# Performance work log

Measured on AMD Instinct MI355X. Metric: run time of the kernel, lower is better.

The kernel has to match this reference:

```python
import jax, jax.numpy as jnp
import numpy as np

TOP_K = 4  # router top-k


def setup_inputs() -> dict:
    key = jax.random.key(0)
    ks = jax.random.split(key, 8)
    B, S, D, E, H, HS = 2, 2048, 2048, 16, 1024, 4096
    scaled = lambda k, shape, fan: (jax.random.normal(k, shape, jnp.float32) * (fan ** -0.5))
    return {
        "x": jax.random.normal(ks[0], (B, S, D), jnp.float32),
        "w_router": scaled(ks[1], (D, E), D),
        # per-expert SwiGLU MLP weights
        "we1": scaled(ks[2], (E, D, H), D),
        "we3": scaled(ks[3], (E, D, H), D),
        "we2": scaled(ks[4], (E, H, D), H),
        # shared SwiGLU MLP weights
        "ws1": scaled(ks[5], (D, HS), D),
        "ws3": scaled(ks[6], (D, HS), D),
        "ws2": scaled(ks[7], (HS, D), HS),
    }


def reference(x, w_router, we1, we3, we2, ws1, ws3, ws2):
    B, S, D = x.shape
    T = B * S
    E = w_router.shape[1]
    xt = x.reshape(T, D)

    # ---- router: softmax over experts, top-k, renormalize top-k weights ----
    probs = jax.nn.softmax(xt @ w_router, axis=-1)           # [T, E]
    top_w, top_i = jax.lax.top_k(probs, TOP_K)               # [T, K]
    top_w = top_w / jnp.sum(top_w, axis=-1, keepdims=True)
    # dense combine weights [T, E] (zero for non-selected experts)
    cw = jnp.zeros((T, E), xt.dtype).at[jnp.arange(T)[:, None], top_i].add(top_w)

    # ---- experts: per-expert SwiGLU, combine with routing weights ----
    g = jax.nn.silu(jnp.einsum("td,edh->teh", xt, we1)) * jnp.einsum("td,edh->teh", xt, we3)
    g = g * cw[:, :, None]                                   # fold combine weight in
    moe_out = jnp.einsum("teh,ehd->td", g, we2)              # [T, D]

    # ---- shared MLP (SwiGLU) and blend ----
    shared = (jax.nn.silu(xt @ ws1) * (xt @ ws3)) @ ws2      # [T, D]
    k = TOP_K
    out = shared / (k + 1) + moe_out * (k / (k + 1))
    return out.reshape(B, S, D)
```

## Files before the change

### kernel.cpp

```cpp
#include <hip/hip_runtime.h>
#include <stdint.h>

#define TTOK  4096
#define DDIM  2048
#define NEXP  16
#define HDIM  1024
#define HSDIM 4096
#define CAPR  18432

typedef __bf16 bf16x8 __attribute__((ext_vector_type(8)));
typedef float  f32x4  __attribute__((ext_vector_type(4)));

__device__ __forceinline__ unsigned short f2b(float f) {
  union { float f; unsigned int i; } v; v.f = f;
  unsigned int r = (v.i + 0x7fffu + ((v.i >> 16) & 1u)) >> 16;
  return (unsigned short)r;
}
__device__ __forceinline__ float b2f(unsigned short u) {
  union { unsigned int i; float f; } v; v.i = ((unsigned int)u) << 16; return v.f;
}
__device__ __forceinline__ float silu_f(float x) { return x / (1.f + __expf(-x)); }

__device__ __forceinline__ void gload16(const void* g, void* l) {
  __builtin_amdgcn_global_load_lds(
      (const __attribute__((address_space(1))) unsigned int*)(uintptr_t)g,
      (__attribute__((address_space(3))) unsigned int*)(uintptr_t)l,
      16, 0, 0);
}

__global__ void cvt_bf16_kernel(const float* __restrict__ in, unsigned short* __restrict__ out, int n8) {
  int i = blockIdx.x * 256 + threadIdx.x;
  if (i >= n8) return;
  const float4* p = (const float4*)in + (size_t)i * 2;
  float4 a = p[0], b = p[1];
  uint4 o;
  o.x = (unsigned)f2b(a.x) | ((unsigned)f2b(a.y) << 16);
  o.y = (unsigned)f2b(a.z) | ((unsigned)f2b(a.w) << 16);
  o.z = (unsigned)f2b(b.x) | ((unsigned)f2b(b.y) << 16);
  o.w = (unsigned)f2b(b.z) | ((unsigned)f2b(b.w) << 16);
  ((uint4*)out)[i] = o;
}

__global__ void transpose_f2b(const float* __restrict__ in, unsigned short* __restrict__ out, int R, int C) {
  __shared__ unsigned short t[64][66];
  size_t zo = (size_t)blockIdx.z * R * C;
  int c0 = blockIdx.x * 64, r0 = blockIdx.y * 64;
  int x = threadIdx.x & 63, y = threadIdx.x >> 6;
#pragma unroll
  for (int j = 0; j < 16; ++j) {
    int r = y * 16 + j;
    t[x][r] = f2b(in[zo + (size_t)(r0 + r) * C + c0 + x]);
  }
  __syncthreads();
#pragma unroll
  for (int j = 0; j < 16; ++j) {
    int c = y * 16 + j;
    out[zo + (size_t)(c0 + c) * R + r0 + x] = t[c][x];
  }
}

__global__ __launch_bounds__(256) void router_kernel(const float* __restrict__ x, const float* __restrict__ wr,
                                                     float* __restrict__ topw, int* __restrict__ topi) {
  int tok = blockIdx.x * 4 + (threadIdx.x >> 6);
  int lane = threadIdx.x & 63;
  const float* xr = x + (size_t)tok * DDIM;
  float acc[NEXP];
#pragma unroll
  for (int e = 0; e < NEXP; ++e) acc[e] = 0.f;
  for (int it = 0; it < DDIM / 64; ++it) {
    int d = it * 64 + lane;
    float xv = xr[d];
    const float4* w4 = (const float4*)(wr + (size_t)d * NEXP);
    float4 w0 = w4[0], w1 = w4[1], w2 = w4[2], w3 = w4[3];
    acc[0] += xv * w0.x; acc[1] += xv * w0.y; acc[2] += xv * w0.z; acc[3] += xv * w0.w;
    acc[4] += xv * w1.x; acc[5] += xv * w1.y; acc[6] += xv * w1.z; acc[7] += xv * w1.w;
    acc[8] += xv * w2.x; acc[9] += xv * w2.y; acc[10] += xv * w2.z; acc[11] += xv * w2.w;
    acc[12] += xv * w3.x; acc[13] += xv * w3.y; acc[14] += xv * w3.z; acc[15] += xv * w3.w;
  }
#pragma unroll
  for (int e = 0; e < NEXP; ++e) {
#pragma unroll
    for (int off = 32; off > 0; off >>= 1) acc[e] += __shfl_xor(acc[e], off);
  }
  unsigned used = 0u;
  float lv[4]; int si[4];
#pragma unroll
  for (int k = 0; k < 4; ++k) {
    float best = -3.4e38f; int bi = 0;
    for (int e = 0; e < NEXP; ++e) {
      if (!((used >> e) & 1u) && acc[e] > best) { best = acc[e]; bi = e; }
    }
    used |= 1u << bi; lv[k] = best; si[k] = bi;
  }
  if (lane == 0) {
    float m = lv[0], s = 0.f, w[4];
#pragma unroll
    for (int k = 0; k < 4; ++k) { w[k] = __expf(lv[k] - m); s += w[k]; }
    float inv = 1.f / s;
#pragma unroll
    for (int k = 0; k < 4; ++k) { topw[tok * 4 + k] = w[k] * inv; topi[tok * 4 + k] = si[k]; }
  }
}

__global__ void zero_kernel(int* b) { if (threadIdx.x < 64) b[threadIdx.x] = 0; }

__global__ void count_kernel(const int* __restrict__ topi, int* counts, int n) {
  int i = blockIdx.x * 256 + threadIdx.x;
  if (i < n) atomicAdd(&counts[topi[i]], 1);
}

__global__ void offsets_kernel(const int* counts, int* eoff) {
  if (threadIdx.x == 0 && blockIdx.x == 0) {
    int o = 0;
    for (int e = 0; e < NEXP; ++e) { eoff[e] = o; o += (counts[e] + 127) & ~127; }
    eoff[NEXP] = o;
  }
}

__global__ void prefill_kernel(int* gtok, float* gwt, int cap) {
  int i = blockIdx.x * 256 + threadIdx.x;
  if (i < cap) { gtok[i] = 0; gwt[i] = 0.f; }
}

__global__ void scatter_kernel(const int* __restrict__ topi, const float* __restrict__ topw,
                               const int* __restrict__ eoff, int* cursors,
                               int* gtok, float* gwt, int* posmap, int n) {
  int i = blockIdx.x * 256 + threadIdx.x;
  if (i >= n) return;
  int e = topi[i];
  int pos = eoff[e] + atomicAdd(&cursors[e], 1);
  gtok[pos] = i >> 2;
  gwt[pos] = topw[i] * 0.8f;
  posmap[i] = pos;
}

__global__ void silu_mul_kernel(const unsigned short* __restrict__ a, const unsigned short* __restrict__ b,
                                unsigned short* __restrict__ g, int n8) {
  int i = blockIdx.x * 256 + threadIdx.x;
  if (i >= n8) return;
  uint4 va = ((const uint4*)a)[i];
  uint4 vb = ((const uint4*)b)[i];
  uint4 vo;
  unsigned* pa = (unsigned*)&va; unsigned* pb = (unsigned*)&vb; unsigned* po = (unsigned*)&vo;
#pragma unroll
  for (int w = 0; w < 4; ++w) {
    float a0 = b2f((unsigned short)(pa[w] & 0xffffu)), a1 = b2f((unsigned short)(pa[w] >> 16));
    float b0 = b2f((unsigned short)(pb[w] & 0xffffu)), b1 = b2f((unsigned short)(pb[w] >> 16));
    float g0 = silu_f(a0) * b0, g1 = silu_f(a1) * b1;
    po[w] = (unsigned)f2b(g0) | ((unsigned)f2b(g1) << 16);
  }
  ((uint4*)g)[i] = vo;
}

__global__ void silu_mul_w_kernel(const unsigned short* __restrict__ a, const unsigned short* __restrict__ b,
                                  const float* __restrict__ gw, unsigned short* __restrict__ g, int n8) {
  int i = blockIdx.x * 256 + threadIdx.x;
  if (i >= n8) return;
  float wrow = gw[i >> 7];
  uint4 va = ((const uint4*)a)[i];
  uint4 vb = ((const uint4*)b)[i];
  uint4 vo;
  unsigned* pa = (unsigned*)&va; unsigned* pb = (unsigned*)&vb; unsigned* po = (unsigned*)&vo;
#pragma unroll
  for (int w = 0; w < 4; ++w) {
    float a0 = b2f((unsigned short)(pa[w] & 0xffffu)), a1 = b2f((unsigned short)(pa[w] >> 16));
    float b0 = b2f((unsigned short)(pb[w] & 0xffffu)), b1 = b2f((unsigned short)(pb[w] >> 16));
    float g0 = silu_f(a0) * b0 * wrow, g1 = silu_f(a1) * b1 * wrow;
    po[w] = (unsigned)f2b(g0) | ((unsigned)f2b(g1) << 16);
  }
  ((uint4*)g)[i] = vo;
}

__global__ __launch_bounds__(256) void combine_kernel(const unsigned short* __restrict__ ecout,
                                                      const int* __restrict__ posmap,
                                                      float* __restrict__ out, int n8) {
  int i = blockIdx.x * 256 + threadIdx.x;
  if (i >= n8) return;
  int t = i >> 8;
  int c = i & 255;
  int4 pv = *(const int4*)&posmap[t * 4];
  float s[8];
  float4 o0 = ((const float4*)out)[(size_t)i * 2];
  float4 o1 = ((const float4*)out)[(size_t)i * 2 + 1];
  s[0]=o0.x; s[1]=o0.y; s[2]=o0.z; s[3]=o0.w; s[4]=o1.x; s[5]=o1.y; s[6]=o1.z; s[7]=o1.w;
  int pos[4] = {pv.x, pv.y, pv.z, pv.w};
#pragma unroll
  for (int k = 0; k < 4; ++k) {
    uint4 v = ((const uint4*)(ecout + (size_t)pos[k] * DDIM))[c];
    unsigned* pw = (unsigned*)&v;
#pragma unroll
    for (int w = 0; w < 4; ++w) {
      s[w * 2]     += b2f((unsigned short)(pw[w] & 0xffffu));
      s[w * 2 + 1] += b2f((unsigned short)(pw[w] >> 16));
    }
  }
  float4 r0 = {s[0], s[1], s[2], s[3]}, r1 = {s[4], s[5], s[6], s[7]};
  ((float4*)out)[(size_t)i * 2] = r0;
  ((float4*)out)[(size_t)i * 2 + 1] = r1;
}

template <int MODE>
__global__ __launch_bounds__(256) void gemm_bt(const unsigned short* __restrict__ A,
                                               const unsigned short* __restrict__ Bt,
                                               unsigned short* __restrict__ Cbf,
                                               float* __restrict__ Cf,
                                               int N, int K,
                                               const int* __restrict__ gtok,
                                               const int* __restrict__ eoff,
                                               float scale) {
  __shared__ unsigned short sA[128 * 64];
  __shared__ unsigned short sB[128 * 64];
  __shared__ int sIdx[128];

  int m0 = blockIdx.x * 128;
  int n0 = blockIdx.y * 128;
  const unsigned short* Bte = Bt;
  if constexpr (MODE == 2 || MODE == 4) {
    if (m0 >= eoff[NEXP]) return;
    int e = 0;
    while (m0 >= eoff[e + 1]) ++e;
    Bte = Bt + (size_t)e * N * K;
  }
  int tid = threadIdx.x;
  int lane = tid & 63;
  int wv = tid >> 6;
  if constexpr (MODE == 2) {
    if (tid < 128) sIdx[tid] = gtok[m0 + tid];
    __syncthreads();
  }
  f32x4 acc[4][4];
#pragma unroll
  for (int mi = 0; mi < 4; ++mi)
#pragma unroll
    for (int ni = 0; ni < 4; ++ni) acc[mi][ni] = (f32x4){0.f, 0.f, 0.f, 0.f};

  int wm = wv >> 1, wn = wv & 1;

  for (int kt = 0; kt < K; kt += 64) {
#pragma unroll
    for (int c = 0; c < 4; ++c) {
      int bofs = (wv * 4 + c) * 1024 + lane * 16;
      int row = bofs >> 7;
      int sch = ((bofs >> 4) & 7) ^ (row & 7);
      int ar;
      if constexpr (MODE == 2) ar = sIdx[row]; else ar = m0 + row;
      gload16(A + (size_t)ar * K + kt + sch * 8, &sA[(wv * 4 + c) * 512]);
      gload16(Bte + (size_t)(n0 + row) * K + kt + sch * 8, &sB[(wv * 4 + c) * 512]);
    }
    __syncthreads();
#pragma unroll
    for (int kk = 0; kk < 2; ++kk) {
      bf16x8 af[4], bfv[4];
#pragma unroll
      for (int mi = 0; mi < 4; ++mi) {
        int row = wm * 64 + mi * 16 + (lane & 15);
        int ch = (kk * 4 + (lane >> 4)) ^ (row & 7);
        af[mi] = *(const bf16x8*)&sA[row * 64 + ch * 8];
      }
#pragma unroll
      for (int ni = 0; ni < 4; ++ni) {
        int row = wn * 64 + ni * 16 + (lane & 15);
        int ch = (kk * 4 + (lane >> 4)) ^ (row & 7);
        bfv[ni] = *(const bf16x8*)&sB[row * 64 + ch * 8];
      }
#pragma unroll
      for (int mi = 0; mi < 4; ++mi)
#pragma unroll
        for (int ni = 0; ni < 4; ++ni)
          acc[mi][ni] = __builtin_amdgcn_mfma_f32_16x16x32_bf16(af[mi], bfv[ni], acc[mi][ni], 0, 0, 0);
    }
    __syncthreads();
  }

#pragma unroll
  for (int mi = 0; mi < 4; ++mi) {
#pragma unroll
    for (int ni = 0; ni < 4; ++ni) {
      int cc = n0 + wn * 64 + ni * 16 + (lane & 15);
#pragma unroll
      for (int j = 0; j < 4; ++j) {
        int rr = m0 + wm * 64 + mi * 16 + ((lane >> 4) << 2) + j;
        float v = acc[mi][ni][j];
        if constexpr (MODE == 1) {
          Cf[(size_t)rr * N + cc] = v * scale;
        } else {
          Cbf[(size_t)rr * N + cc] = f2b(v);
        }
      }
    }
  }
}

extern "C" void kernel_launch(void* const* d_in, const int* in_sizes, int n_in,
                              void* d_out, int out_size, void* d_ws, size_t ws_size,
                              hipStream_t stream) {
  const float* x   = (const float*)d_in[0];
  const float* wr  = (const float*)d_in[1];
  const float* we1 = (const float*)d_in[2];
  const float* we3 = (const float*)d_in[3];
  const float* we2 = (const float*)d_in[4];
  const float* ws1 = (const float*)d_in[5];
  const float* ws3 = (const float*)d_in[6];
  const float* ws2 = (const float*)d_in[7];
  float* out = (float*)d_out;

  char* p = (char*)d_ws;
  auto take = [&](size_t bytes) { char* r = p; p += (bytes + 255) & ~(size_t)255; return r; };
  unsigned short* xbf = (unsigned short*)take((size_t)TTOK * DDIM * 2);
  unsigned short* eh1 = (unsigned short*)take((size_t)CAPR * HDIM * 2);
  unsigned short* h1  = (unsigned short*)take((size_t)TTOK * HSDIM * 2);
  unsigned short* h3  = (unsigned short*)take((size_t)TTOK * HSDIM * 2);
  unsigned short* eh3 = (unsigned short*)take((size_t)CAPR * HDIM * 2);
  unsigned short* tw  = (unsigned short*)take((size_t)NEXP * HDIM * DDIM * 2);
  float* topw = (float*)take((size_t)TTOK * 4 * 4);
  int*   topi = (int*)take((size_t)TTOK * 4 * 4);
  int*   gtok = (int*)take((size_t)CAPR * 4);
  float* gwt  = (float*)take((size_t)CAPR * 4);
  int*   posmap = (int*)take((size_t)TTOK * 4 * 4);
  int*   ibuf = (int*)take(256);
  if ((size_t)(p - (char*)d_ws) > ws_size) return;

  unsigned short* ecout = h1;

  int* counts  = ibuf;
  int* cursors = ibuf + 16;
  int* eoff    = ibuf + 32;

  cvt_bf16_kernel<<<TTOK * DDIM / 8 / 256, 256, 0, stream>>>(x, xbf, TTOK * DDIM / 8);
  router_kernel<<<TTOK / 4, 256, 0, stream>>>(x, wr, topw, topi);
  zero_kernel<<<1, 64, 0, stream>>>(ibuf);
  count_kernel<<<TTOK * 4 / 256, 256, 0, stream>>>(topi, counts, TTOK * 4);
  offsets_kernel<<<1, 64, 0, stream>>>(counts, eoff);
  prefill_kernel<<<CAPR / 256, 256, 0, stream>>>(gtok, gwt, CAPR);
  scatter_kernel<<<TTOK * 4 / 256, 256, 0, stream>>>(topi, topw, eoff, cursors, gtok, gwt, posmap, TTOK * 4);

  transpose_f2b<<<dim3(HSDIM / 64, DDIM / 64, 1), 256, 0, stream>>>(ws1, tw, DDIM, HSDIM);
  gemm_bt<0><<<dim3(TTOK / 128, HSDIM / 128), 256, 0, stream>>>(xbf, tw, h1, nullptr, HSDIM, DDIM, nullptr, nullptr, 0.f);
  transpose_f2b<<<dim3(HSDIM / 64, DDIM / 64, 1), 256, 0, stream>>>(ws3, tw, DDIM, HSDIM);
  gemm_bt<0><<<dim3(TTOK / 128, HSDIM / 128), 256, 0, stream>>>(xbf, tw, h3, nullptr, HSDIM, DDIM, nullptr, nullptr, 0.f);
  silu_mul_kernel<<<TTOK * HSDIM / 8 / 256, 256, 0, stream>>>(h1, h3, h1, TTOK * HSDIM / 8);
  transpose_f2b<<<dim3(DDIM / 64, HSDIM / 64, 1), 256, 0, stream>>>(ws2, tw, HSDIM, DDIM);
  gemm_bt<1><<<dim3(TTOK / 128, DDIM / 128), 256, 0, stream>>>(h1, tw, nullptr, out, DDIM, HSDIM, nullptr, nullptr, 0.2f);

  transpose_f2b<<<dim3(HDIM / 64, DDIM / 64, NEXP), 256, 0, stream>>>(we1, tw, DDIM, HDIM);
  gemm_bt<2><<<dim3(CAPR / 128, HDIM / 128), 256, 0, stream>>>(xbf, tw, eh1, nullptr, HDIM, DDIM, gtok, eoff, 0.f);
  transpose_f2b<<<dim3(HDIM / 64, DDIM / 64, NEXP), 256, 0, stream>>>(we3, tw, DDIM, HDIM);
  gemm_bt<2><<<dim3(CAPR / 128, HDIM / 128), 256, 0, stream>>>(xbf, tw, eh3, nullptr, HDIM, DDIM, gtok, eoff, 0.f);
  silu_mul_w_kernel<<<CAPR * HDIM / 8 / 256, 256, 0, stream>>>(eh1, eh3, gwt, eh1, CAPR * HDIM / 8);
  transpose_f2b<<<dim3(DDIM / 64, HDIM / 64, NEXP), 256, 0, stream>>>(we2, tw, HDIM, DDIM);
  gemm_bt<4><<<dim3(CAPR / 128, DDIM / 128), 256, 0, stream>>>(eh1, tw, ecout, nullptr, DDIM, HDIM, nullptr, eoff, 0.f);

  combine_kernel<<<TTOK * DDIM / 8 / 256, 256, 0, stream>>>(ecout, posmap, out, TTOK * DDIM / 8);
}
```

Baseline: 939.0 us.

## Replace 128x128 GEMM with double-buffered 256x256 pipelined MFMA kernel

Swaps the single-buffered 128x128-tile GEMM for a 256x256-tile, 512-thread kernel. It double-buffers LDS, interleaves async global-to-LDS loads with MFMA phases using explicit waitcnt, barriers and setprio, and remaps workgroups across XCDs. Expert capacity padding grows to 256-row multiples, so the grouped-GEMM buffers are enlarged. The aim is to hide memory latency and raise per-tile data reuse. The cost is more padded expert rows, higher register and LDS pressure, and fragile hand-tuned scheduling.

```diff
diff --git a/kernel.cpp b/kernel.cpp
--- a/kernel.cpp
+++ b/kernel.cpp
@@ -6,7 +6,7 @@
 #define NEXP  16
 #define HDIM  1024
 #define HSDIM 4096
-#define CAPR  18432
+#define CAPR2 20480
 
 typedef __bf16 bf16x8 __attribute__((ext_vector_type(8)));
 typedef float  f32x4  __attribute__((ext_vector_type(4)));
@@ -112,7 +112,7 @@
 __global__ void offsets_kernel(const int* counts, int* eoff) {
   if (threadIdx.x == 0 && blockIdx.x == 0) {
     int o = 0;
-    for (int e = 0; e < NEXP; ++e) { eoff[e] = o; o += (counts[e] + 127) & ~127; }
+    for (int e = 0; e < NEXP; ++e) { eoff[e] = o; o += (counts[e] + 255) & ~255; }
     eoff[NEXP] = o;
   }
 }
@@ -199,96 +199,138 @@
   ((float4*)out)[(size_t)i * 2 + 1] = r1;
 }
 
+
+#define STAGE_A(b, h, kt) do { \
+  gload16(Aptr + (size_t)rA[h][0]*K + (size_t)(kt)*64 + schEl, (char*)sA[b] + (h)*16384 + wv*1024); \
+  gload16(Aptr + (size_t)rA[h][1]*K + (size_t)(kt)*64 + schEl, (char*)sA[b] + (h)*16384 + 8192 + wv*1024); \
+} while (0)
+
+#define STAGE_B(b, h, kt) do { \
+  gload16(Bte + (size_t)rB[h][0]*K + (size_t)(kt)*64 + schEl, (char*)sB[b] + (h)*16384 + wv*1024); \
+  gload16(Bte + (size_t)rB[h][1]*K + (size_t)(kt)*64 + schEl, (char*)sB[b] + (h)*16384 + 8192 + wv*1024); \
+} while (0)
+
+#define PHASE(QA, QB, BUF, VM, ...) do { \
+  bf16x8 af[4][2], bfr[2][2]; \
+  _Pragma("unroll") for (int mi = 0; mi < 4; ++mi) { \
+    const int row_ = (QA)*128 + wr*64 + mi*16 + (lane & 15); \
+    _Pragma("unroll") for (int kk = 0; kk < 2; ++kk) { \
+      const int ch_ = (kk*4 + (lane>>4)) ^ (row_ & 7); \
+      af[mi][kk] = *(const bf16x8*)&sA[BUF][row_*64 + ch_*8]; } } \
+  _Pragma("unroll") for (int ni = 0; ni < 2; ++ni) { \
+    const int row_ = (QB)*128 + wc*32 + ni*16 + (lane & 15); \
+    _Pragma("unroll") for (int kk = 0; kk < 2; ++kk) { \
+      const int ch_ = (kk*4 + (lane>>4)) ^ (row_ & 7); \
+      bfr[ni][kk] = *(const bf16x8*)&sB[BUF][row_*64 + ch_*8]; } } \
+  __VA_ARGS__ \
+  if ((VM) == 4) { asm volatile("s_waitcnt vmcnt(4)" ::: "memory"); } \
+  else if ((VM) == 0) { asm volatile("s_waitcnt vmcnt(0)" ::: "memory"); } \
+  __builtin_amdgcn_sched_barrier(0); \
+  __builtin_amdgcn_s_barrier(); \
+  __builtin_amdgcn_sched_barrier(0); \
+  __builtin_amdgcn_s_setprio(1); \
+  _Pragma("unroll") for (int mi = 0; mi < 4; ++mi) \
+    _Pragma("unroll") for (int ni = 0; ni < 2; ++ni) \
+      _Pragma("unroll") for (int kk = 0; kk < 2; ++kk) \
+        acc[QA][QB][mi][ni] = __builtin_amdgcn_mfma_f32_16x16x32_bf16(af[mi][kk], bfr[ni][kk], acc[QA][QB][mi][ni], 0, 0, 0); \
+  __builtin_amdgcn_s_setprio(0); \
+  __builtin_amdgcn_sched_barrier(0); \
+  __builtin_amdgcn_s_barrier(); \
+  __builtin_amdgcn_sched_barrier(0); \
+} while (0)
+
 template <int MODE>
-__global__ __launch_bounds__(256) void gemm_bt(const unsigned short* __restrict__ A,
-                                               const unsigned short* __restrict__ Bt,
-                                               unsigned short* __restrict__ Cbf,
-                                               float* __restrict__ Cf,
-                                               int N, int K,
-                                               const int* __restrict__ gtok,
-                                               const int* __restrict__ eoff,
-                                               float scale) {
-  __shared__ unsigned short sA[128 * 64];
-  __shared__ unsigned short sB[128 * 64];
-  __shared__ int sIdx[128];
-
-  int m0 = blockIdx.x * 128;
-  int n0 = blockIdx.y * 128;
+__global__ __launch_bounds__(512, 2) void gemm256(const unsigned short* __restrict__ Aptr,
+                                                  const unsigned short* __restrict__ Bt,
+                                                  unsigned short* __restrict__ Cbf,
+                                                  float* __restrict__ Cf,
+                                                  int N, int K, int MB,
+                                                  const int* __restrict__ gtok,
+                                                  const int* __restrict__ eoff,
+                                                  float scale) {
+  __shared__ unsigned short sA[2][256 * 64];
+  __shared__ unsigned short sB[2][256 * 64];
+
+  int nwg = gridDim.x;
+  int q = nwg >> 3, r = nwg & 7;
+  int xcd = blockIdx.x & 7, off = blockIdx.x >> 3;
+  int wg = (xcd < r ? xcd * (q + 1) : r * (q + 1) + (xcd - r) * q) + off;
+  int m0 = (wg % MB) * 256;
+  int n0 = (wg / MB) * 256;
+
   const unsigned short* Bte = Bt;
   if constexpr (MODE == 2 || MODE == 4) {
     if (m0 >= eoff[NEXP]) return;
     int e = 0;
     while (m0 >= eoff[e + 1]) ++e;
-    Bte = Bt + (size_t)e * N * K;
-  }
-  int tid = threadIdx.x;
-  int lane = tid & 63;
-  int wv = tid >> 6;
-  if constexpr (MODE == 2) {
-    if (tid < 128) sIdx[tid] = gtok[m0 + tid];
-    __syncthreads();
-  }
-  f32x4 acc[4][4];
-#pragma unroll
-  for (int mi = 0; mi < 4; ++mi)
-#pragma unroll
-    for (int ni = 0; ni < 4; ++ni) acc[mi][ni] = (f32x4){0.f, 0.f, 0.f, 0.f};
-
-  int wm = wv >> 1, wn = wv & 1;
-
-  for (int kt = 0; kt < K; kt += 64) {
-#pragma unroll
-    for (int c = 0; c < 4; ++c) {
-      int bofs = (wv * 4 + c) * 1024 + lane * 16;
-      int row = bofs >> 7;
-      int sch = ((bofs >> 4) & 7) ^ (row & 7);
-      int ar;
-      if constexpr (MODE == 2) ar = sIdx[row]; else ar = m0 + row;
-      gload16(A + (size_t)ar * K + kt + sch * 8, &sA[(wv * 4 + c) * 512]);
-      gload16(Bte + (size_t)(n0 + row) * K + kt + sch * 8, &sB[(wv * 4 + c) * 512]);
+    Bte += (size_t)e * N * K;
+  }
+
+  int tid = threadIdx.x, lane = tid & 63, wv = tid >> 6;
+  int wr = wv >> 2, wc = wv & 3;
+  const int schEl = ((lane & 7) ^ (lane >> 3)) * 8;
+  int rA[2][2], rB[2][2];
+#pragma unroll
+  for (int h = 0; h < 2; ++h)
+#pragma unroll
+    for (int s = 0; s < 2; ++s) {
+      int row = h * 128 + s * 64 + wv * 8 + (lane >> 3);
+      rB[h][s] = n0 + row;
+      if constexpr (MODE == 2) rA[h][s] = gtok[m0 + row];
+      else rA[h][s] = m0 + row;
     }
-    __syncthreads();
-#pragma unroll
-    for (int kk = 0; kk < 2; ++kk) {
-      bf16x8 af[4], bfv[4];
-#pragma unroll
-      for (int mi = 0; mi < 4; ++mi) {
-        int row = wm * 64 + mi * 16 + (lane & 15);
-        int ch = (kk * 4 + (lane >> 4)) ^ (row & 7);
-        af[mi] = *(const bf16x8*)&sA[row * 64 + ch * 8];
-      }
-#pragma unroll
-      for (int ni = 0; ni < 4; ++ni) {
-        int row = wn * 64 + ni * 16 + (lane & 15);
-        int ch = (kk * 4 + (lane >> 4)) ^ (row & 7);
-        bfv[ni] = *(const bf16x8*)&sB[row * 64 + ch * 8];
-      }
+
+  f32x4 acc[2][2][4][2];
+#pragma unroll
+  for (int a_ = 0; a_ < 2; ++a_)
+#pragma unroll
+    for (int b_ = 0; b_ < 2; ++b_)
 #pragma unroll
       for (int mi = 0; mi < 4; ++mi)
 #pragma unroll
-        for (int ni = 0; ni < 4; ++ni)
-          acc[mi][ni] = __builtin_amdgcn_mfma_f32_16x16x32_bf16(af[mi], bfv[ni], acc[mi][ni], 0, 0, 0);
-    }
-    __syncthreads();
-  }
-
-#pragma unroll
-  for (int mi = 0; mi < 4; ++mi) {
-#pragma unroll
-    for (int ni = 0; ni < 4; ++ni) {
-      int cc = n0 + wn * 64 + ni * 16 + (lane & 15);
-#pragma unroll
-      for (int j = 0; j < 4; ++j) {
-        int rr = m0 + wm * 64 + mi * 16 + ((lane >> 4) << 2) + j;
-        float v = acc[mi][ni][j];
-        if constexpr (MODE == 1) {
-          Cf[(size_t)rr * N + cc] = v * scale;
-        } else {
-          Cbf[(size_t)rr * N + cc] = f2b(v);
+        for (int ni = 0; ni < 2; ++ni) acc[a_][b_][mi][ni] = (f32x4){0.f, 0.f, 0.f, 0.f};
+
+  STAGE_A(0, 0, 0); STAGE_B(0, 0, 0); STAGE_A(0, 1, 0); STAGE_B(0, 1, 0);
+  __builtin_amdgcn_sched_barrier(0);
+  STAGE_A(1, 0, 1); STAGE_B(1, 0, 1); STAGE_A(1, 1, 1); STAGE_B(1, 1, 1);
+  asm volatile("s_waitcnt vmcnt(8)" ::: "memory");
+  __builtin_amdgcn_sched_barrier(0);
+  __builtin_amdgcn_s_barrier();
+  __builtin_amdgcn_sched_barrier(0);
+
+  int NI = K >> 7;
+  for (int j = 0; j < NI; ++j) {
+    int kt1 = 2 * j + 1;
+    bool pre = (j + 1 < NI), post = (j > 0);
+    int vmTail = pre ? 4 : 0;
+    PHASE(0, 0, 0, -1, if (post) { STAGE_A(1, 1, kt1); STAGE_B(1, 1, kt1); });
+    PHASE(0, 1, 0, -1, ;);
+    PHASE(1, 0, 0, -1, if (pre) { STAGE_A(0, 0, kt1 + 1); });
+    PHASE(1, 1, 0, vmTail, if (pre) { STAGE_B(0, 0, kt1 + 1); });
+    PHASE(0, 0, 1, -1, if (pre) { STAGE_A(0, 1, kt1 + 1); STAGE_B(0, 1, kt1 + 1); });
+    PHASE(0, 1, 1, -1, ;);
+    PHASE(1, 0, 1, -1, if (pre) { STAGE_A(1, 0, kt1 + 2); });
+    PHASE(1, 1, 1, vmTail, if (pre) { STAGE_B(1, 0, kt1 + 2); });
+  }
+
+  asm volatile("" ::: "memory");
+#pragma unroll
+  for (int qa = 0; qa < 2; ++qa)
+#pragma unroll
+    for (int qb = 0; qb < 2; ++qb)
+#pragma unroll
+      for (int mi = 0; mi < 4; ++mi)
+#pragma unroll
+        for (int ni = 0; ni < 2; ++ni) {
+          int cc = n0 + qb * 128 + wc * 32 + ni * 16 + (lane & 15);
+#pragma unroll
+          for (int jj = 0; jj < 4; ++jj) {
+            int rr = m0 + qa * 128 + wr * 64 + mi * 16 + ((lane >> 4) << 2) + jj;
+            float v = acc[qa][qb][mi][ni][jj];
+            if constexpr (MODE == 1) Cf[(size_t)rr * N + cc] = v * scale;
+            else Cbf[(size_t)rr * N + cc] = f2b(v);
+          }
         }
-      }
-    }
-  }
 }
 
 extern "C" void kernel_launch(void* const* d_in, const int* in_sizes, int n_in,
@@ -307,15 +349,15 @@
   char* p = (char*)d_ws;
   auto take = [&](size_t bytes) { char* r = p; p += (bytes + 255) & ~(size_t)255; return r; };
   unsigned short* xbf = (unsigned short*)take((size_t)TTOK * DDIM * 2);
-  unsigned short* eh1 = (unsigned short*)take((size_t)CAPR * HDIM * 2);
+  unsigned short* eh1 = (unsigned short*)take((size_t)CAPR2 * HDIM * 2);
   unsigned short* h1  = (unsigned short*)take((size_t)TTOK * HSDIM * 2);
   unsigned short* h3  = (unsigned short*)take((size_t)TTOK * HSDIM * 2);
-  unsigned short* eh3 = (unsigned short*)take((size_t)CAPR * HDIM * 2);
+  unsigned short* eh3 = (unsigned short*)take((size_t)CAPR2 * HDIM * 2);
   unsigned short* tw  = (unsigned short*)take((size_t)NEXP * HDIM * DDIM * 2);
   float* topw = (float*)take((size_t)TTOK * 4 * 4);
   int*   topi = (int*)take((size_t)TTOK * 4 * 4);
-  int*   gtok = (int*)take((size_t)CAPR * 4);
-  float* gwt  = (float*)take((size_t)CAPR * 4);
+  int*   gtok = (int*)take((size_t)CAPR2 * 4);
+  float* gwt  = (float*)take((size_t)CAPR2 * 4);
   int*   posmap = (int*)take((size_t)TTOK * 4 * 4);
   int*   ibuf = (int*)take(256);
   if ((size_t)(p - (char*)d_ws) > ws_size) return;
@@ -331,24 +373,24 @@
   zero_kernel<<<1, 64, 0, stream>>>(ibuf);
   count_kernel<<<TTOK * 4 / 256, 256, 0, stream>>>(topi, counts, TTOK * 4);
   offsets_kernel<<<1, 64, 0, stream>>>(counts, eoff);
-  prefill_kernel<<<CAPR / 256, 256, 0, stream>>>(gtok, gwt, CAPR);
+  prefill_kernel<<<CAPR2 / 256, 256, 0, stream>>>(gtok, gwt, CAPR2);
   scatter_kernel<<<TTOK * 4 / 256, 256, 0, stream>>>(topi, topw, eoff, cursors, gtok, gwt, posmap, TTOK * 4);
 
   transpose_f2b<<<dim3(HSDIM / 64, DDIM / 64, 1), 256, 0, stream>>>(ws1, tw, DDIM, HSDIM);
-  gemm_bt<0><<<dim3(TTOK / 128, HSDIM / 128), 256, 0, stream>>>(xbf, tw, h1, nullptr, HSDIM, DDIM, nullptr, nullptr, 0.f);
+  gemm256<0><<<(TTOK / 256) * (HSDIM / 256), 512, 0, stream>>>(xbf, tw, h1, nullptr, HSDIM, DDIM, TTOK / 256, nullptr, nullptr, 0.f);
   transpose_f2b<<<dim3(HSDIM / 64, DDIM / 64, 1), 256, 0, stream>>>(ws3, tw, DDIM, HSDIM);
-  gemm_bt<0><<<dim3(TTOK / 128, HSDIM / 128), 256, 0, stream>>>(xbf, tw, h3, nullptr, HSDIM, DDIM, nullptr, nullptr, 0.f);
+  gemm256<0><<<(TTOK / 256) * (HSDIM / 256), 512, 0, stream>>>(xbf, tw, h3, nullptr, HSDIM, DDIM, TTOK / 256, nullptr, nullptr, 0.f);
   silu_mul_kernel<<<TTOK * HSDIM / 8 / 256, 256, 0, stream>>>(h1, h3, h1, TTOK * HSDIM / 8);
   transpose_f2b<<<dim3(DDIM / 64, HSDIM / 64, 1), 256, 0, stream>>>(ws2, tw, HSDIM, DDIM);
-  gemm_bt<1><<<dim3(TTOK / 128, DDIM / 128), 256, 0, stream>>>(h1, tw, nullptr, out, DDIM, HSDIM, nullptr, nullptr, 0.2f);
+  gemm256<1><<<(TTOK / 256) * (DDIM / 256), 512, 0, stream>>>(h1, tw, nullptr, out, DDIM, HSDIM, TTOK / 256, nullptr, nullptr, 0.2f);
 
   transpose_f2b<<<dim3(HDIM / 64, DDIM / 64, NEXP), 256, 0, stream>>>(we1, tw, DDIM, HDIM);
-  gemm_bt<2><<<dim3(CAPR / 128, HDIM / 128), 256, 0, stream>>>(xbf, tw, eh1, nullptr, HDIM, DDIM, gtok, eoff, 0.f);
+  gemm256<2><<<(CAPR2 / 256) * (HDIM / 256), 512, 0, stream>>>(xbf, tw, eh1, nullptr, HDIM, DDIM, CAPR2 / 256, gtok, eoff, 0.f);
   transpose_f2b<<<dim3(HDIM / 64, DDIM / 64, NEXP), 256, 0, stream>>>(we3, tw, DDIM, HDIM);
-  gemm_bt<2><<<dim3(CAPR / 128, HDIM / 128), 256, 0, stream>>>(xbf, tw, eh3, nullptr, HDIM, DDIM, gtok, eoff, 0.f);
-  silu_mul_w_kernel<<<CAPR * HDIM / 8 / 256, 256, 0, stream>>>(eh1, eh3, gwt, eh1, CAPR * HDIM / 8);
+  gemm256<2><<<(CAPR2 / 256) * (HDIM / 256), 512, 0, stream>>>(xbf, tw, eh3, nullptr, HDIM, DDIM, CAPR2 / 256, gtok, eoff, 0.f);
+  silu_mul_w_kernel<<<CAPR2 * HDIM / 8 / 256, 256, 0, stream>>>(eh1, eh3, gwt, eh1, CAPR2 * HDIM / 8);
   transpose_f2b<<<dim3(DDIM / 64, HDIM / 64, NEXP), 256, 0, stream>>>(we2, tw, HDIM, DDIM);
-  gemm_bt<4><<<dim3(CAPR / 128, DDIM / 128), 256, 0, stream>>>(eh1, tw, ecout, nullptr, DDIM, HDIM, nullptr, eoff, 0.f);
+  gemm256<4><<<(CAPR2 / 256) * (DDIM / 256), 512, 0, stream>>>(eh1, tw, ecout, nullptr, DDIM, HDIM, CAPR2 / 256, nullptr, eoff, 0.f);
 
   combine_kernel<<<TTOK * DDIM / 8 / 256, 256, 0, stream>>>(ecout, posmap, out, TTOK * DDIM / 8);
 }
```

Result: no change. 929.4 us (-1.0%).

## Fuse gate/up GEMMs with SiLU epilogue and add XCD-aware block swizzle

Applied to the files above, without the earlier changes.

Adds a dual-weight GEMM kernel that computes the W1 and W3 projections in one pass over the A tile and applies SiLU, the multiply and the routing weight in the epilogue. This replaces the separate gate GEMM, up GEMM and silu_mul kernels for both the shared and the expert MLPs. Expert weights are now transposed in two halves of eight experts so they fit a split weight arena. The grids become 1D with an XCD-aware block remapping intended to improve L2 locality. The cost is higher register and LDS use per block with 512 threads, and the expert path now needs two launches.

```diff
diff --git a/kernel.cpp b/kernel.cpp
--- a/kernel.cpp
+++ b/kernel.cpp
@@ -26,6 +26,12 @@
       (const __attribute__((address_space(1))) unsigned int*)(uintptr_t)g,
       (__attribute__((address_space(3))) unsigned int*)(uintptr_t)l,
       16, 0, 0);
+}
+
+__device__ __forceinline__ int xcd_swz(int bid, int nwg) {
+  int q = nwg >> 3, r = nwg & 7;
+  int xcd = bid & 7, off = bid >> 3;
+  return (xcd < r ? xcd * (q + 1) : r * (q + 1) + (xcd - r) * q) + off;
 }
 
 __global__ void cvt_bf16_kernel(const float* __restrict__ in, unsigned short* __restrict__ out, int n8) {
@@ -132,43 +138,6 @@
   gtok[pos] = i >> 2;
   gwt[pos] = topw[i] * 0.8f;
   posmap[i] = pos;
-}
-
-__global__ void silu_mul_kernel(const unsigned short* __restrict__ a, const unsigned short* __restrict__ b,
-                                unsigned short* __restrict__ g, int n8) {
-  int i = blockIdx.x * 256 + threadIdx.x;
-  if (i >= n8) return;
-  uint4 va = ((const uint4*)a)[i];
-  uint4 vb = ((const uint4*)b)[i];
-  uint4 vo;
-  unsigned* pa = (unsigned*)&va; unsigned* pb = (unsigned*)&vb; unsigned* po = (unsigned*)&vo;
-#pragma unroll
-  for (int w = 0; w < 4; ++w) {
-    float a0 = b2f((unsigned short)(pa[w] & 0xffffu)), a1 = b2f((unsigned short)(pa[w] >> 16));
-    float b0 = b2f((unsigned short)(pb[w] & 0xffffu)), b1 = b2f((unsigned short)(pb[w] >> 16));
-    float g0 = silu_f(a0) * b0, g1 = silu_f(a1) * b1;
-    po[w] = (unsigned)f2b(g0) | ((unsigned)f2b(g1) << 16);
-  }
-  ((uint4*)g)[i] = vo;
-}
-
-__global__ void silu_mul_w_kernel(const unsigned short* __restrict__ a, const unsigned short* __restrict__ b,
-                                  const float* __restrict__ gw, unsigned short* __restrict__ g, int n8) {
-  int i = blockIdx.x * 256 + threadIdx.x;
-  if (i >= n8) return;
-  float wrow = gw[i >> 7];
-  uint4 va = ((const uint4*)a)[i];
-  uint4 vb = ((const uint4*)b)[i];
-  uint4 vo;
-  unsigned* pa = (unsigned*)&va; unsigned* pb = (unsigned*)&vb; unsigned* po = (unsigned*)&vo;
-#pragma unroll
-  for (int w = 0; w < 4; ++w) {
-    float a0 = b2f((unsigned short)(pa[w] & 0xffffu)), a1 = b2f((unsigned short)(pa[w] >> 16));
-    float b0 = b2f((unsigned short)(pb[w] & 0xffffu)), b1 = b2f((unsigned short)(pb[w] >> 16));
-    float g0 = silu_f(a0) * b0 * wrow, g1 = silu_f(a1) * b1 * wrow;
-    po[w] = (unsigned)f2b(g0) | ((unsigned)f2b(g1) << 16);
-  }
-  ((uint4*)g)[i] = vo;
 }
 
 __global__ __launch_bounds__(256) void combine_kernel(const unsigned short* __restrict__ ecout,
@@ -200,34 +169,127 @@
 }
 
 template <int MODE>
+__global__ __launch_bounds__(512) void gemm_dual(const unsigned short* __restrict__ A,
+                                                 const unsigned short* __restrict__ W1,
+                                                 const unsigned short* __restrict__ W3,
+                                                 unsigned short* __restrict__ G,
+                                                 int N, int K, int MB,
+                                                 const int* __restrict__ gtok,
+                                                 const float* __restrict__ gwt,
+                                                 const int* __restrict__ eoff,
+                                                 int eBase) {
+  __shared__ unsigned short sA[128 * 64];
+  __shared__ unsigned short s1[128 * 64];
+  __shared__ unsigned short s3[128 * 64];
+  __shared__ int sIdx[128];
+
+  int wg = xcd_swz(blockIdx.x, gridDim.x);
+  int m0 = (wg % MB) * 128;
+  int n0 = (wg / MB) * 128;
+
+  const unsigned short* W1e = W1;
+  const unsigned short* W3e = W3;
+  if constexpr (MODE == 2) {
+    m0 += eoff[eBase];
+    if (m0 >= eoff[eBase + 8]) return;
+    int e = eBase;
+    while (m0 >= eoff[e + 1]) ++e;
+    size_t wofs = (size_t)(e - eBase) * N * K;
+    W1e += wofs; W3e += wofs;
+  }
+
+  int tid = threadIdx.x, lane = tid & 63, wv = tid >> 6;
+  if constexpr (MODE == 2) {
+    if (tid < 128) sIdx[tid] = gtok[m0 + tid];
+    __syncthreads();
+  }
+
+  int wm = wv >> 2, wn = wv & 3;
+  f32x4 ac1[4][2], ac3[4][2];
+#pragma unroll
+  for (int mi = 0; mi < 4; ++mi)
+#pragma unroll
+    for (int ni = 0; ni < 2; ++ni) { ac1[mi][ni] = (f32x4){0,0,0,0}; ac3[mi][ni] = (f32x4){0,0,0,0}; }
+
+  for (int kt = 0; kt < K; kt += 64) {
+#pragma unroll
+    for (int c = 0; c < 2; ++c) {
+      int bofs = (wv * 2 + c) * 1024 + lane * 16;
+      int row = bofs >> 7;
+      int sch = ((bofs >> 4) & 7) ^ (row & 7);
+      int ar;
+      if constexpr (MODE == 2) ar = sIdx[row]; else ar = m0 + row;
+      gload16(A   + (size_t)ar * K        + kt + sch * 8, &sA[(wv * 2 + c) * 512]);
+      gload16(W1e + (size_t)(n0 + row) * K + kt + sch * 8, &s1[(wv * 2 + c) * 512]);
+      gload16(W3e + (size_t)(n0 + row) * K + kt + sch * 8, &s3[(wv * 2 + c) * 512]);
+    }
+    __syncthreads();
+#pragma unroll
+    for (int kk = 0; kk < 2; ++kk) {
+      bf16x8 af[4], b1[2], b3[2];
+#pragma unroll
+      for (int mi = 0; mi < 4; ++mi) {
+        int row = wm * 64 + mi * 16 + (lane & 15);
+        int ch = (kk * 4 + (lane >> 4)) ^ (row & 7);
+        af[mi] = *(const bf16x8*)&sA[row * 64 + ch * 8];
+      }
+#pragma unroll
+      for (int ni = 0; ni < 2; ++ni) {
+        int row = wn * 32 + ni * 16 + (lane & 15);
+        int ch = (kk * 4 + (lane >> 4)) ^ (row & 7);
+        b1[ni] = *(const bf16x8*)&s1[row * 64 + ch * 8];
+        b3[ni] = *(const bf16x8*)&s3[row * 64 + ch * 8];
+      }
+#pragma unroll
+      for (int mi = 0; mi < 4; ++mi)
+#pragma unroll
+        for (int ni = 0; ni < 2; ++ni) {
+          ac1[mi][ni] = __builtin_amdgcn_mfma_f32_16x16x32_bf16(af[mi], b1[ni], ac1[mi][ni], 0, 0, 0);
+          ac3[mi][ni] = __builtin_amdgcn_mfma_f32_16x16x32_bf16(af[mi], b3[ni], ac3[mi][ni], 0, 0, 0);
+        }
+    }
+    __syncthreads();
+  }
+
+#pragma unroll
+  for (int mi = 0; mi < 4; ++mi)
+#pragma unroll
+    for (int ni = 0; ni < 2; ++ni) {
+      int cc = n0 + wn * 32 + ni * 16 + (lane & 15);
+#pragma unroll
+      for (int j = 0; j < 4; ++j) {
+        int rr = m0 + wm * 64 + mi * 16 + ((lane >> 4) << 2) + j;
+        float sc;
+        if constexpr (MODE == 2) sc = gwt[rr]; else sc = 1.f;
+        float g = silu_f(ac1[mi][ni][j]) * ac3[mi][ni][j] * sc;
+        G[(size_t)rr * N + cc] = f2b(g);
+      }
+    }
+}
+
+template <int MODE>
 __global__ __launch_bounds__(256) void gemm_bt(const unsigned short* __restrict__ A,
                                                const unsigned short* __restrict__ Bt,
                                                unsigned short* __restrict__ Cbf,
                                                float* __restrict__ Cf,
-                                               int N, int K,
-                                               const int* __restrict__ gtok,
+                                               int N, int K, int MB,
                                                const int* __restrict__ eoff,
                                                float scale) {
   __shared__ unsigned short sA[128 * 64];
   __shared__ unsigned short sB[128 * 64];
-  __shared__ int sIdx[128];
-
-  int m0 = blockIdx.x * 128;
-  int n0 = blockIdx.y * 128;
+
+  int wg = xcd_swz(blockIdx.x, gridDim.x);
+  int m0 = (wg % MB) * 128;
+  int n0 = (wg / MB) * 128;
+
   const unsigned short* Bte = Bt;
-  if constexpr (MODE == 2 || MODE == 4) {
+  if constexpr (MODE == 4) {
     if (m0 >= eoff[NEXP]) return;
     int e = 0;
     while (m0 >= eoff[e + 1]) ++e;
     Bte = Bt + (size_t)e * N * K;
   }
-  int tid = threadIdx.x;
-  int lane = tid & 63;
-  int wv = tid >> 6;
-  if constexpr (MODE == 2) {
-    if (tid < 128) sIdx[tid] = gtok[m0 + tid];
-    __syncthreads();
-  }
+  int tid = threadIdx.x, lane = tid & 63, wv = tid >> 6;
   f32x4 acc[4][4];
 #pragma unroll
   for (int mi = 0; mi < 4; ++mi)
@@ -242,9 +304,7 @@
       int bofs = (wv * 4 + c) * 1024 + lane * 16;
       int row = bofs >> 7;
       int sch = ((bofs >> 4) & 7) ^ (row & 7);
-      int ar;
-      if constexpr (MODE == 2) ar = sIdx[row]; else ar = m0 + row;
-      gload16(A + (size_t)ar * K + kt + sch * 8, &sA[(wv * 4 + c) * 512]);
+      gload16(A   + (size_t)(m0 + row) * K + kt + sch * 8, &sA[(wv * 4 + c) * 512]);
       gload16(Bte + (size_t)(n0 + row) * K + kt + sch * 8, &sB[(wv * 4 + c) * 512]);
     }
     __syncthreads();
@@ -273,7 +333,7 @@
   }
 
 #pragma unroll
-  for (int mi = 0; mi < 4; ++mi) {
+  for (int mi = 0; mi < 4; ++mi)
 #pragma unroll
     for (int ni = 0; ni < 4; ++ni) {
       int cc = n0 + wn * 64 + ni * 16 + (lane & 15);
@@ -281,14 +341,10 @@
       for (int j = 0; j < 4; ++j) {
         int rr = m0 + wm * 64 + mi * 16 + ((lane >> 4) << 2) + j;
         float v = acc[mi][ni][j];
-        if constexpr (MODE == 1) {
-          Cf[(size_t)rr * N + cc] = v * scale;
-        } else {
-          Cbf[(size_t)rr * N + cc] = f2b(v);
-        }
-      }
-    }
-  }
+        if constexpr (MODE == 1) Cf[(size_t)rr * N + cc] = v * scale;
+        else Cbf[(size_t)rr * N + cc] = f2b(v);
+      }
+    }
 }
 
 extern "C" void kernel_launch(void* const* d_in, const int* in_sizes, int n_in,
@@ -306,12 +362,11 @@
 
   char* p = (char*)d_ws;
   auto take = [&](size_t bytes) { char* r = p; p += (bytes + 255) & ~(size_t)255; return r; };
-  unsigned short* xbf = (unsigned short*)take((size_t)TTOK * DDIM * 2);
-  unsigned short* eh1 = (unsigned short*)take((size_t)CAPR * HDIM * 2);
-  unsigned short* h1  = (unsigned short*)take((size_t)TTOK * HSDIM * 2);
-  unsigned short* h3  = (unsigned short*)take((size_t)TTOK * HSDIM * 2);
-  unsigned short* eh3 = (unsigned short*)take((size_t)CAPR * HDIM * 2);
-  unsigned short* tw  = (unsigned short*)take((size_t)NEXP * HDIM * DDIM * 2);
+  unsigned short* xbf   = (unsigned short*)take((size_t)TTOK * DDIM * 2);
+  unsigned short* ehg   = (unsigned short*)take((size_t)CAPR * HDIM * 2);
+  unsigned short* gsh   = (unsigned short*)take((size_t)TTOK * HSDIM * 2);
+  unsigned short* ecout = (unsigned short*)take((size_t)CAPR * DDIM * 2);
+  unsigned short* twArena = (unsigned short*)take((size_t)NEXP * HDIM * DDIM * 2);
   float* topw = (float*)take((size_t)TTOK * 4 * 4);
   int*   topi = (int*)take((size_t)TTOK * 4 * 4);
   int*   gtok = (int*)take((size_t)CAPR * 4);
@@ -320,7 +375,8 @@
   int*   ibuf = (int*)take(256);
   if ((size_t)(p - (char*)d_ws) > ws_size) return;
 
-  unsigned short* ecout = h1;
+  unsigned short* twA = twArena;
+  unsigned short* twB = twArena + (size_t)8 * DDIM * HDIM;
 
   int* counts  = ibuf;
   int* cursors = ibuf + 16;
@@ -334,21 +390,25 @@
   prefill_kernel<<<CAPR / 256, 256, 0, stream>>>(gtok, gwt, CAPR);
   scatter_kernel<<<TTOK * 4 / 256, 256, 0, stream>>>(topi, topw, eoff, cursors, gtok, gwt, posmap, TTOK * 4);
 
-  transpose_f2b<<<dim3(HSDIM / 64, DDIM / 64, 1), 256, 0, stream>>>(ws1, tw, DDIM, HSDIM);
-  gemm_bt<0><<<dim3(TTOK / 128, HSDIM / 128), 256, 0, stream>>>(xbf, tw, h1, nullptr, HSDIM, DDIM, nullptr, nullptr, 0.f);
-  transpose_f2b<<<dim3(HSDIM / 64, DDIM / 64, 1), 256, 0, stream>>>(ws3, tw, DDIM, HSDIM);
-  gemm_bt<0><<<dim3(TTOK / 128, HSDIM / 128), 256, 0, stream>>>(xbf, tw, h3, nullptr, HSDIM, DDIM, nullptr, nullptr, 0.f);
-  silu_mul_kernel<<<TTOK * HSDIM / 8 / 256, 256, 0, stream>>>(h1, h3, h1, TTOK * HSDIM / 8);
-  transpose_f2b<<<dim3(DDIM / 64, HSDIM / 64, 1), 256, 0, stream>>>(ws2, tw, HSDIM, DDIM);
-  gemm_bt<1><<<dim3(TTOK / 128, DDIM / 128), 256, 0, stream>>>(h1, tw, nullptr, out, DDIM, HSDIM, nullptr, nullptr, 0.2f);
-
-  transpose_f2b<<<dim3(HDIM / 64, DDIM / 64, NEXP), 256, 0, stream>>>(we1, tw, DDIM, HDIM);
-  gemm_bt<2><<<dim3(CAPR / 128, HDIM / 128), 256, 0, stream>>>(xbf, tw, eh1, nullptr, HDIM, DDIM, gtok, eoff, 0.f);
-  transpose_f2b<<<dim3(HDIM / 64, DDIM / 64, NEXP), 256, 0, stream>>>(we3, tw, DDIM, HDIM);
-  gemm_bt<2><<<dim3(CAPR / 128, HDIM / 128), 256, 0, stream>>>(xbf, tw, eh3, nullptr, HDIM, DDIM, gtok, eoff, 0.f);
-  silu_mul_w_kernel<<<CAPR * HDIM / 8 / 256, 256, 0, stream>>>(eh1, eh3, gwt, eh1, CAPR * HDIM / 8);
-  transpose_f2b<<<dim3(DDIM / 64, HDIM / 64, NEXP), 256, 0, stream>>>(we2, tw, HDIM, DDIM);
-  gemm_bt<4><<<dim3(CAPR / 128, DDIM / 128), 256, 0, stream>>>(eh1, tw, ecout, nullptr, DDIM, HDIM, nullptr, eoff, 0.f);
+  transpose_f2b<<<dim3(HSDIM / 64, DDIM / 64, 1), 256, 0, stream>>>(ws1, twA, DDIM, HSDIM);
+  transpose_f2b<<<dim3(HSDIM / 64, DDIM / 64, 1), 256, 0, stream>>>(ws3, twB, DDIM, HSDIM);
+  gemm_dual<0><<<(TTOK / 128) * (HSDIM / 128), 512, 0, stream>>>(xbf, twA, twB, gsh, HSDIM, DDIM,
+                                                                 TTOK / 128, nullptr, nullptr, nullptr, 0);
+  transpose_f2b<<<dim3(DDIM / 64, HSDIM / 64, 1), 256, 0, stream>>>(ws2, twA, HSDIM, DDIM);
+  gemm_bt<1><<<(TTOK / 128) * (DDIM / 128), 256, 0, stream>>>(gsh, twA, nullptr, out, DDIM, HSDIM,
+                                                              TTOK / 128, nullptr, 0.2f);
+
+  for (int h = 0; h < 2; ++h) {
+    const float* w1h = we1 + (size_t)h * 8 * DDIM * HDIM;
+    const float* w3h = we3 + (size_t)h * 8 * DDIM * HDIM;
+    transpose_f2b<<<dim3(HDIM / 64, DDIM / 64, 8), 256, 0, stream>>>(w1h, twA, DDIM, HDIM);
+    transpose_f2b<<<dim3(HDIM / 64, DDIM / 64, 8), 256, 0, stream>>>(w3h, twB, DDIM, HDIM);
+    gemm_dual<2><<<(CAPR / 128) * (HDIM / 128), 512, 0, stream>>>(xbf, twA, twB, ehg, HDIM, DDIM,
+                                                                  CAPR / 128, gtok, gwt, eoff, 8 * h);
+  }
+  transpose_f2b<<<dim3(DDIM / 64, HDIM / 64, NEXP), 256, 0, stream>>>(we2, twArena, HDIM, DDIM);
+  gemm_bt<4><<<(CAPR / 128) * (DDIM / 128), 256, 0, stream>>>(ehg, twArena, ecout, nullptr, DDIM, HDIM,
+                                                              CAPR / 128, eoff, 0.f);
 
   combine_kernel<<<TTOK * DDIM / 8 / 256, 256, 0, stream>>>(ecout, posmap, out, TTOK * DDIM / 8);
 }
```

Measured after the change: 820.5 us. 1.14x faster.
